# Kernel tuning notes

Measured on AMD Instinct MI355X. Metric: run time of the kernel, lower is better.

The kernel has to match this reference:

```python
import jax, jax.numpy as jnp
import numpy as np

PT_SEQ_LEN = 16    # hardcoded hw_seq_len in the module
THETA = 10000.0


def _rope_tables(head_dim):
    # VisionRotaryEmbeddingFast with dim = head_dim // 2, pt_seq_len = ft_seq_len = 16
    d = head_dim // 2                                   # 32
    freqs = 1.0 / (THETA ** (np.arange(0, d, 2, dtype=np.float64) / d))  # (d//2,) = (16,)
    t = np.arange(PT_SEQ_LEN, dtype=np.float64)         # t / ft * pt = arange since ft==pt
    f = np.einsum('i,j->ij', t, freqs)                  # (16, 16)
    f = np.repeat(f, 2, axis=-1)                        # (16, 32)  '... n -> ... (n r)'
    fa = np.broadcast_to(f[:, None, :], (PT_SEQ_LEN, PT_SEQ_LEN, d))
    fb = np.broadcast_to(f[None, :, :], (PT_SEQ_LEN, PT_SEQ_LEN, d))
    full = np.concatenate([fa, fb], axis=-1).reshape(-1, head_dim)  # (256, head_dim)
    return (jnp.asarray(np.cos(full), dtype=jnp.float32),
            jnp.asarray(np.sin(full), dtype=jnp.float32))


def _rotate_half(x):
    # '... (d r) -> ... d r', r=2; (x1, x2) -> (-x2, x1)
    x = x.reshape(*x.shape[:-1], -1, 2)
    x1, x2 = x[..., 0], x[..., 1]
    return jnp.stack((-x2, x1), axis=-1).reshape(*x.shape[:-2], -1)


def _apply_rope(t, cos, sin):
    # t: (B, H, N, hd); cos/sin: (N, hd)
    return t * cos + _rotate_half(t) * sin


def setup_inputs() -> dict:
    key = jax.random.key(0)
    ks = jax.random.split(key, 5)
    B, N, dim, sem = 64, 256, 1024, 768
    return {
        'q': jax.random.normal(ks[0], (B, N, dim), dtype=jnp.float32),
        'kv': jax.random.normal(ks[1], (B, N, sem), dtype=jnp.float32),
        'Wq': jax.random.normal(ks[2], (dim, dim), dtype=jnp.float32) * 0.02,
        'Wkv': jax.random.normal(ks[3], (sem, 2 * dim), dtype=jnp.float32) * 0.02,
        'Wproj': jax.random.normal(ks[4], (dim, dim), dtype=jnp.float32) * 0.02,
        'bproj': jnp.zeros((dim,), dtype=jnp.float32),
    }


def reference(q, kv, Wq, Wkv, Wproj, bproj):
    B, N, C = q.shape
    H = 16
    hd = C // H
    cos, sin = _rope_tables(hd)

    qh = (q @ Wq).reshape(B, N, H, hd).transpose(0, 2, 1, 3)        # (B,H,N,hd)
    kvh = (kv @ Wkv).reshape(B, N, 2, H, hd).transpose(2, 0, 3, 1, 4)
    k, v = kvh[0], kvh[1]                                           # (B,H,N,hd)

    qh = _apply_rope(qh, cos, sin)
    k = _apply_rope(k, cos, sin)

    scale = 1.0 / jnp.sqrt(jnp.float32(hd))  # F.sdpa default scale
    logits = jnp.einsum('bhqd,bhkd->bhqk', qh, k) * scale
    attn = jax.nn.softmax(logits, axis=-1)
    out = jnp.einsum('bhqk,bhkd->bhqd', attn, v)                    # (B,H,N,hd)
    out = out.transpose(0, 2, 1, 3).reshape(B, N, C)
    return out @ Wproj + bproj
```

## Files before the change

### kernel.cpp

```cpp
#include <hip/hip_runtime.h>
#include <hip/hip_bf16.h>
#include <math.h>


typedef unsigned int uint;
typedef __attribute__((ext_vector_type(4)))  short s16x4;
typedef __attribute__((ext_vector_type(8)))  short s16x8;
typedef __attribute__((ext_vector_type(4)))  float f32x4;

#define AS1 __attribute__((address_space(1)))
#define AS3 __attribute__((address_space(3)))

__device__ __forceinline__ short f2bf(float x){
  union{float f;uint u;}v; v.f=x;
  return (short)((v.u + 0x7FFFu + ((v.u>>16)&1u))>>16);
}
__device__ __forceinline__ float bf2f(short s){
  union{float f;uint u;}v; v.u=((uint)(unsigned short)s)<<16; return v.f;
}
__device__ __forceinline__ uint packbf(float a,float b){
  return (uint)(unsigned short)f2bf(a) | ((uint)(unsigned short)f2bf(b)<<16);
}
__device__ __forceinline__ void gl_lds16(const void* g, void* l){
  __builtin_amdgcn_global_load_lds((const AS1 uint*)g, (AS3 uint*)l, 16, 0, 0);
}
__device__ __forceinline__ s16x8 ld16(const short* p){ return *(const s16x8*)p; }

__global__ void k_detect(const uint* q, int* flag){
  __shared__ int cnt;
  if(threadIdx.x==0) cnt=0;
  __syncthreads();
  int c=0;
  for(int i=threadIdx.x;i<4096;i+=256){
    uint e=(q[i]>>7)&0xFFu;
    if(e>=120u && e<=130u) c++;
  }
  atomicAdd(&cnt,c);
  __syncthreads();
  if(threadIdx.x==0) *flag = (cnt>2048)?0:1;
}

__global__ void k_convert(const void* src, short* dst, long n8, const int* flag){
  int f=*flag;
  long stride=(long)gridDim.x*blockDim.x;
  for(long i=(long)blockIdx.x*blockDim.x+threadIdx.x;i<n8;i+=stride){
    s16x8 o;
    if(f){
      const float4* s=(const float4*)src;
      float4 a=s[i*2], b=s[i*2+1];
      o[0]=f2bf(a.x);o[1]=f2bf(a.y);o[2]=f2bf(a.z);o[3]=f2bf(a.w);
      o[4]=f2bf(b.x);o[5]=f2bf(b.y);o[6]=f2bf(b.z);o[7]=f2bf(b.w);
    }else{
      o=((const s16x8*)src)[i];
    }
    ((s16x8*)dst)[i]=o;
  }
}

__global__ void k_transpose(const void* W, short* WT, int K, int Nn, const int* flag){
  int f=*flag;
  long total=(long)Nn*(K/8);
  long stride=(long)gridDim.x*blockDim.x;
  for(long idx=(long)blockIdx.x*blockDim.x+threadIdx.x;idx<total;idx+=stride){
    int n=(int)(idx%Nn); int kc=(int)(idx/Nn); int k0=kc*8;
    s16x8 o;
    #pragma unroll
    for(int j=0;j<8;j++){
      o[j]= f ? f2bf(((const float*)W)[(long)(k0+j)*Nn+n])
              : ((const short*)W)[(long)(k0+j)*Nn+n];
    }
    *(s16x8*)&WT[(long)n*K+k0]=o;
  }
}

__global__ void k_tables(float* cosT, float* sinT){
  int t=blockIdx.x*blockDim.x+threadIdx.x;
  if(t>=256*64) return;
  int n=t>>6, d=t&63;
  int i=n>>4, j=n&15;
  int p=(d&31)>>1;
  double fr=pow(10000.0, -(double)(2*p)/32.0);
  double tt=(d<32)?(double)i:(double)j;
  double a=tt*fr;
  cosT[t]=(float)cos(a);
  sinT[t]=(float)sin(a);
}

__global__ void k_bias(const void* b, float* bo, const int* flag){
  int t=blockIdx.x*blockDim.x+threadIdx.x;
  if(t<1024) bo[t] = (*flag)? ((const float*)b)[t] : bf2f(((const short*)b)[t]);
}

template<int EPI>
__launch_bounds__(256,2)
__global__ void k_gemm(const short* A, const short* BT, int Kdim,
                       short* out0, short* out1,
                       const float* cosT, const float* sinT,
                       const float* bias, const int* flag, void* dout){
  __shared__ __align__(16) short Alds[2][128*32];
  __shared__ __align__(16) short Blds[2][128*32];
  const int tid=threadIdx.x, lane=tid&63;
  const int wave=tid>>6, wm=wave>>1, wn=wave&1;
  const int tn=blockIdx.x, tm=blockIdx.y;
  const int fl=*flag;
  f32x4 acc[4][4]={};
  const short* Ag=A+(long)tm*128*Kdim;
  const short* Bg=BT+(long)tn*128*Kdim;
  const int row0=tid>>2, c0=tid&3;
  const int row1=64+row0;
  const int sw0=(c0^((row0>>1)&3))*8;
  const int sw1=(c0^((row1>>1)&3))*8;

  #define STAGE(bufsel,kb) do{                                        \
    gl_lds16(Ag+(long)row0*Kdim+(kb)+sw0, &Alds[bufsel][tid*8]);      \
    gl_lds16(Ag+(long)row1*Kdim+(kb)+sw1, &Alds[bufsel][(256+tid)*8]);\
    gl_lds16(Bg+(long)row0*Kdim+(kb)+sw0, &Blds[bufsel][tid*8]);      \
    gl_lds16(Bg+(long)row1*Kdim+(kb)+sw1, &Blds[bufsel][(256+tid)*8]);\
  }while(0)

  const int nt=Kdim>>5;
  STAGE(0,0);
  __syncthreads();
  int cur=0;
  for(int t=0;t<nt;t++){
    if(t+1<nt) STAGE(cur^1,(t+1)*32);
    s16x8 af[4], bfr[4];
    #pragma unroll
    for(int rb=0;rb<4;rb++){
      int ar=wm*64+rb*16+(lane&15);
      af[rb]=*(const s16x8*)&Alds[cur][ar*32+(((lane>>4)^((ar>>1)&3))*8)];
    }
    #pragma unroll
    for(int cb=0;cb<4;cb++){
      int br=wn*64+cb*16+(lane&15);
      bfr[cb]=*(const s16x8*)&Blds[cur][br*32+(((lane>>4)^((br>>1)&3))*8)];
    }
    #pragma unroll
    for(int rb=0;rb<4;rb++)
      #pragma unroll
      for(int cb=0;cb<4;cb++)
        acc[rb][cb]=__builtin_amdgcn_mfma_f32_16x16x32_bf16(af[rb],bfr[cb],acc[rb][cb],0,0,0);
    __syncthreads();
    cur^=1;
  }
  #undef STAGE

  const int mbase=tm*128+wm*64, nbase=tn*128+wn*64;
  const int g=lane>>4, li=lane&15;
  #pragma unroll
  for(int rb=0;rb<4;rb++)
  #pragma unroll
  for(int cb=0;cb<4;cb++){
    const int m0=mbase+rb*16+g*4;
    const int n=nbase+cb*16+li;
    if(EPI==0){
      #pragma unroll
      for(int r=0;r<4;r++){
        float v=acc[rb][cb][r];
        int m=m0+r; int b=m>>8, nn=m&255, h=n>>6, d=n&63;
        float part=__shfl_xor(v,1);
        float c=cosT[(nn<<6)+d], s=sinT[(nn<<6)+d];
        float rot=(d&1)?part:-part;
        out0[(((long)(b*16+h)*256+nn)<<6)+d]=f2bf((v*c+rot*s)*0.125f);
      }
    } else if(EPI==1){
      if(n<1024){
        #pragma unroll
        for(int r=0;r<4;r++){
          float v=acc[rb][cb][r];
          int m=m0+r; int b=m>>8, nn=m&255, h=(n>>6)&15, d=n&63;
          float part=__shfl_xor(v,1);
          float c=cosT[(nn<<6)+d], s=sinT[(nn<<6)+d];
          float rot=(d&1)?part:-part;
          out0[(((long)(b*16+h)*256+nn)<<6)+d]=f2bf(v*c+rot*s);
        }
      }else{
        int h=(n>>6)&15, d=n&63;
        int b=m0>>8, nn0=m0&255;
        s16x4 pk;
        #pragma unroll
        for(int r=0;r<4;r++) pk[r]=f2bf(acc[rb][cb][r]);
        *(s16x4*)&out1[(((long)(b*16+h)*64+d)<<8)+nn0]=pk;
      }
    } else {
      #pragma unroll
      for(int r=0;r<4;r++){
        float o=acc[rb][cb][r]+bias[n];
        long idx=((long)(m0+r)<<10)+n;
        if(fl) ((float*)dout)[idx]=o;
        else   ((short*)dout)[idx]=f2bf(o);
      }
    }
  }
}

__launch_bounds__(256,2)
__global__ void k_attn(const short* qh, const short* kb, const short* vt, short* out){
  __shared__ __align__(16) short ol[4][64][72];
  int bh=blockIdx.x, b=bh>>4, h=bh&15;
  int tid=threadIdx.x, lane=tid&63, wave=tid>>6;
  const short* Q=qh+(long)bh*256*64;
  const short* K=kb+(long)bh*256*64;
  const short* VT=vt+(long)bh*64*256;

  s16x8 qf[4][2];
  #pragma unroll
  for(int qb=0;qb<4;qb++)
    #pragma unroll
    for(int kk=0;kk<2;kk++)
      qf[qb][kk]=ld16(Q+(wave*64+qb*16+(lane&15))*64+kk*32+(lane>>4)*8);

  f32x4 o[4][4]={};
  float mrow[4]={-INFINITY,-INFINITY,-INFINITY,-INFINITY};
  float srow[4]={0.f,0.f,0.f,0.f};
  const int g=lane>>4;
  const int srcA=(lane&15)|((((g<<1))&3)<<4);
  const int srcB=(lane&15)|((((g<<1)|1)&3)<<4);
  const bool hi=(g>=2);

  for(int kt=0;kt<8;kt++){
    s16x8 kA[2][2];
    #pragma unroll
    for(int f=0;f<2;f++)
      #pragma unroll
      for(int kk=0;kk<2;kk++)
        kA[f][kk]=ld16(K+(kt*32+f*16+(lane&15))*64+kk*32+(lane>>4)*8);
    f32x4 st[2][4]={};
    #pragma unroll
    for(int kk=0;kk<2;kk++)
      #pragma unroll
      for(int f=0;f<2;f++)
        #pragma unroll
        for(int qb=0;qb<4;qb++)
          st[f][qb]=__builtin_amdgcn_mfma_f32_16x16x32_bf16(kA[f][kk],qf[qb][kk],st[f][qb],0,0,0);

    s16x8 pb[4];
    #pragma unroll
    for(int qb=0;qb<4;qb++){
      float pm=st[0][qb][0];
      #pragma unroll
      for(int f=0;f<2;f++)
        #pragma unroll
        for(int r=0;r<4;r++) pm=fmaxf(pm,st[f][qb][r]);
      pm=fmaxf(pm,__shfl_xor(pm,16));
      pm=fmaxf(pm,__shfl_xor(pm,32));
      float mn=fmaxf(mrow[qb],pm);
      float al=__expf(mrow[qb]-mn);
      mrow[qb]=mn;
      float p00=__expf(st[0][qb][0]-mn), p01=__expf(st[0][qb][1]-mn);
      float p02=__expf(st[0][qb][2]-mn), p03=__expf(st[0][qb][3]-mn);
      float p10=__expf(st[1][qb][0]-mn), p11=__expf(st[1][qb][1]-mn);
      float p12=__expf(st[1][qb][2]-mn), p13=__expf(st[1][qb][3]-mn);
      float ps=p00+p01+p02+p03+p10+p11+p12+p13;
      ps+=__shfl_xor(ps,16);
      ps+=__shfl_xor(ps,32);
      srow[qb]=srow[qb]*al+ps;
      #pragma unroll
      for(int db=0;db<4;db++){
        o[db][qb][0]*=al; o[db][qb][1]*=al; o[db][qb][2]*=al; o[db][qb][3]*=al;
      }
      uint pk00=packbf(p00,p01), pk01=packbf(p02,p03);
      uint pk10=packbf(p10,p11), pk11=packbf(p12,p13);
      uint s00=(uint)__shfl((int)pk00,srcA), s10=(uint)__shfl((int)pk10,srcA);
      uint s01=(uint)__shfl((int)pk01,srcA), s11=(uint)__shfl((int)pk11,srcA);
      uint t00=(uint)__shfl((int)pk00,srcB), t10=(uint)__shfl((int)pk10,srcB);
      uint t01=(uint)__shfl((int)pk01,srcB), t11=(uint)__shfl((int)pk11,srcB);
      union{s16x8 v;uint u[4];}pp;
      pp.u[0]=hi?s10:s00;
      pp.u[1]=hi?s11:s01;
      pp.u[2]=hi?t10:t00;
      pp.u[3]=hi?t11:t01;
      pb[qb]=pp.v;
    }
    s16x8 vA[4];
    #pragma unroll
    for(int db=0;db<4;db++)
      vA[db]=ld16(VT+(db*16+(lane&15))*256+kt*32+(lane>>4)*8);
    #pragma unroll
    for(int db=0;db<4;db++)
      #pragma unroll
      for(int qb=0;qb<4;qb++)
        o[db][qb]=__builtin_amdgcn_mfma_f32_16x16x32_bf16(vA[db],pb[qb],o[db][qb],0,0,0);
  }

  #pragma unroll
  for(int db=0;db<4;db++)
    #pragma unroll
    for(int qb=0;qb<4;qb++)
      #pragma unroll
      for(int r=0;r<4;r++){
        int d=db*16+(lane>>4)*4+r;
        int q=qb*16+(lane&15);
        ol[wave][q][d]=f2bf(o[db][qb][r]/srow[qb]);
      }
  __syncthreads();
  #pragma unroll
  for(int it=0;it<8;it++){
    int q=wave*64+it*8+(lane>>3);
    int cc=lane&7;
    s16x8 x=*(const s16x8*)&ol[wave][it*8+(lane>>3)][cc*8];
    *(s16x8*)&out[((long)(b*256+q)<<10)+h*64+cc*8]=x;
  }
}

extern "C" void kernel_launch(void* const* d_in, const int* in_sizes, int n_in,
                              void* d_out, int out_size, void* d_ws, size_t ws_size,
                              hipStream_t stream){
  const long M=16384;
  char* ws=(char*)d_ws;
  size_t off=0;
  auto alloc=[&](size_t b){ void* p=ws+off; off+=(b+255)&~(size_t)255; return p; };
  int*   flag =(int*)  alloc(256);
  float* cosT =(float*)alloc(256*64*4);
  float* sinT =(float*)alloc(256*64*4);
  float* biasF=(float*)alloc(1024*4);
  short* qbf  =(short*)alloc((size_t)M*1024*2);
  short* kvbf =(short*)alloc((size_t)M*768*2);
  short* WqT  =(short*)alloc((size_t)1024*1024*2);
  short* WkvT =(short*)alloc((size_t)2048*768*2);
  short* WpT  =(short*)alloc((size_t)1024*1024*2);
  short* qhB  =(short*)alloc((size_t)16777216*2);
  short* kbuf =(short*)alloc((size_t)16777216*2);
  short* vtb  =(short*)alloc((size_t)16777216*2);

  k_detect<<<1,256,0,stream>>>((const uint*)d_in[0],flag);
  k_tables<<<64,256,0,stream>>>(cosT,sinT);
  k_bias<<<4,256,0,stream>>>(d_in[5],biasF,flag);
  k_convert<<<2048,256,0,stream>>>(d_in[0],qbf,(long)M*1024/8,flag);
  k_convert<<<2048,256,0,stream>>>(d_in[1],kvbf,(long)M*768/8,flag);
  k_transpose<<<512,256,0,stream>>>(d_in[2],WqT,1024,1024,flag);
  k_transpose<<<768,256,0,stream>>>(d_in[3],WkvT,768,2048,flag);
  k_transpose<<<512,256,0,stream>>>(d_in[4],WpT,1024,1024,flag);

  k_gemm<0><<<dim3(8,128),256,0,stream>>>(qbf ,WqT ,1024,qhB ,nullptr,cosT,sinT,biasF,flag,nullptr);
  k_gemm<1><<<dim3(16,128),256,0,stream>>>(kvbf,WkvT, 768,kbuf,vtb    ,cosT,sinT,biasF,flag,nullptr);
  k_attn<<<1024,256,0,stream>>>(qhB,kbuf,vtb,qbf);
  k_gemm<2><<<dim3(8,128),256,0,stream>>>(qbf ,WpT ,1024,nullptr,nullptr,cosT,sinT,biasF,flag,d_out);
}
```

Baseline: 310.6 us.

## Replace GEMM with 256x256-tile 8-wave ping-pong pipelined kernel

Replaces the 128x128, 4-wave, K=32 double-buffered GEMM with a 256x256-tile, 8-wave kernel that uses K=64 stages. Global-to-LDS loads of the next tiles are interleaved with MFMA quarter-blocks, using explicit barriers, waitcnt and s_setprio. Workgroups are remapped across the 8 XCDs for L2 locality. The aim is to raise data reuse per LDS byte and overlap memory traffic with compute. In exchange it adds much higher register pressure (128 accumulators per lane), fragile hand-written synchronisation, and a wraparound prefetch past the last K tile.

```diff
diff --git a/kernel.cpp b/kernel.cpp
--- a/kernel.cpp
+++ b/kernel.cpp
@@ -6,6 +6,7 @@
 typedef unsigned int uint;
 typedef __attribute__((ext_vector_type(4)))  short s16x4;
 typedef __attribute__((ext_vector_type(8)))  short s16x8;
+typedef __attribute__((ext_vector_type(16))) short s16x16;
 typedef __attribute__((ext_vector_type(4)))  float f32x4;
 
 #define AS1 __attribute__((address_space(1)))
@@ -91,73 +92,115 @@
   if(t<1024) bo[t] = (*flag)? ((const float*)b)[t] : bf2f(((const short*)b)[t]);
 }
 
+#define BAR   __builtin_amdgcn_s_barrier()
+#define LGKM0 asm volatile("s_waitcnt lgkmcnt(0)" ::: "memory")
+#define VMC4  asm volatile("s_waitcnt vmcnt(4)" ::: "memory")
+#define PRIO1 __builtin_amdgcn_s_setprio(1)
+#define PRIO0 __builtin_amdgcn_s_setprio(0)
+
+#define MM(H,V,BR) do{ \
+  _Pragma("unroll") for(int ks_=0;ks_<2;ks_++){ \
+    _Pragma("unroll") for(int mf_=0;mf_<4;mf_++){ \
+      _Pragma("unroll") for(int nf_=0;nf_<2;nf_++){ \
+        acc[(H)*4+mf_][(V)*2+nf_]=__builtin_amdgcn_mfma_f32_16x16x32_bf16( \
+          aR[mf_][ks_],BR[nf_][ks_],acc[(H)*4+mf_][(V)*2+nf_],0,0,0); \
+  }}} }while(0)
+
+#define HALFIT(BUF,TA,TB) do{ \
+  const short* RA=&lds[BUF][0][wm][0]; \
+  const short* RB=&lds[BUF][1][0][0]; \
+  ldA(RA,0,aR); ldB(RB,0,bR0); stage(0,0,TA); \
+  BAR; LGKM0; PRIO1; MM(0,0,bR0); PRIO0; BAR; \
+  ldB(RB,1,bR1); stage(0,1,TA); \
+  BAR; LGKM0; PRIO1; MM(0,1,bR1); PRIO0; BAR; \
+  ldA(RA,1,aR); stage(1,0,TB); \
+  BAR; LGKM0; PRIO1; MM(1,1,bR1); PRIO0; BAR; \
+  stage(1,1,TB); \
+  BAR; PRIO1; MM(1,0,bR0); PRIO0; VMC4; BAR; \
+}while(0)
+
 template<int EPI>
-__launch_bounds__(256,2)
-__global__ void k_gemm(const short* A, const short* BT, int Kdim,
-                       short* out0, short* out1,
-                       const float* cosT, const float* sinT,
-                       const float* bias, const int* flag, void* dout){
-  __shared__ __align__(16) short Alds[2][128*32];
-  __shared__ __align__(16) short Blds[2][128*32];
-  const int tid=threadIdx.x, lane=tid&63;
-  const int wave=tid>>6, wm=wave>>1, wn=wave&1;
-  const int tn=blockIdx.x, tm=blockIdx.y;
-  const int fl=*flag;
-  f32x4 acc[4][4]={};
-  const short* Ag=A+(long)tm*128*Kdim;
-  const short* Bg=BT+(long)tn*128*Kdim;
-  const int row0=tid>>2, c0=tid&3;
-  const int row1=64+row0;
-  const int sw0=(c0^((row0>>1)&3))*8;
-  const int sw1=(c0^((row1>>1)&3))*8;
-
-  #define STAGE(bufsel,kb) do{                                        \
-    gl_lds16(Ag+(long)row0*Kdim+(kb)+sw0, &Alds[bufsel][tid*8]);      \
-    gl_lds16(Ag+(long)row1*Kdim+(kb)+sw1, &Alds[bufsel][(256+tid)*8]);\
-    gl_lds16(Bg+(long)row0*Kdim+(kb)+sw0, &Blds[bufsel][tid*8]);      \
-    gl_lds16(Bg+(long)row1*Kdim+(kb)+sw1, &Blds[bufsel][(256+tid)*8]);\
-  }while(0)
-
-  const int nt=Kdim>>5;
-  STAGE(0,0);
-  __syncthreads();
-  int cur=0;
-  for(int t=0;t<nt;t++){
-    if(t+1<nt) STAGE(cur^1,(t+1)*32);
-    s16x8 af[4], bfr[4];
-    #pragma unroll
-    for(int rb=0;rb<4;rb++){
-      int ar=wm*64+rb*16+(lane&15);
-      af[rb]=*(const s16x8*)&Alds[cur][ar*32+(((lane>>4)^((ar>>1)&3))*8)];
-    }
-    #pragma unroll
-    for(int cb=0;cb<4;cb++){
-      int br=wn*64+cb*16+(lane&15);
-      bfr[cb]=*(const s16x8*)&Blds[cur][br*32+(((lane>>4)^((br>>1)&3))*8)];
-    }
-    #pragma unroll
-    for(int rb=0;rb<4;rb++)
-      #pragma unroll
-      for(int cb=0;cb<4;cb++)
-        acc[rb][cb]=__builtin_amdgcn_mfma_f32_16x16x32_bf16(af[rb],bfr[cb],acc[rb][cb],0,0,0);
-    __syncthreads();
-    cur^=1;
-  }
-  #undef STAGE
-
-  const int mbase=tm*128+wm*64, nbase=tn*128+wn*64;
-  const int g=lane>>4, li=lane&15;
-  #pragma unroll
-  for(int rb=0;rb<4;rb++)
-  #pragma unroll
-  for(int cb=0;cb<4;cb++){
-    const int m0=mbase+rb*16+g*4;
-    const int n=nbase+cb*16+li;
+__launch_bounds__(512,2)
+__global__ void k_gemm8(const short* __restrict__ A, const short* __restrict__ BT,
+                        const int Kdim, const int lgN,
+                        short* __restrict__ out0, short* __restrict__ out1,
+                        const float* __restrict__ cosT, const float* __restrict__ sinT,
+                        const float* __restrict__ bias, const int* __restrict__ flag,
+                        void* __restrict__ dout){
+  __shared__ __align__(16) short lds[2][2][2][8192];
+  const int tid=threadIdx.x, lane=tid&63, wave=tid>>6;
+  const int li=lane&15, gq=lane>>4;
+  const int wm=wave>>2, wn=wave&3;
+  const int nwg=gridDim.x, cpx=nwg>>3;
+  const int wg=((int)blockIdx.x&7)*cpx+((int)blockIdx.x>>3);
+  const int tn=wg&((1<<lgN)-1), tm=wg>>lgN;
+  const int NT=Kdim>>6;
+  const short* Ag=A+(long)tm*256*Kdim;
+  const short* Bg=BT+(long)tn*256*Kdim;
+  const int fl=(EPI==2)? *flag : 0;
+  f32x4 acc[8][4]={};
+  s16x8 aR[4][2], bR0[2][2], bR1[2][2];
+
+  auto stage=[&](int op,int hf,int kt){
+    int ktw=(kt>=NT)?kt-NT:kt;
+    const short* G=(op? Bg:Ag)+((long)(hf*128))*Kdim+ktw*64;
+    short* R=&lds[kt&1][op][hf][0];
+    #pragma unroll
+    for(int l=0;l<2;l++){
+      int lr=l*64+wave*8+(lane>>3);
+      int c=(lane&7)^((lr>>1)&7);
+      gl_lds16(G+(long)lr*Kdim+c*8, R+l*4096+wave*512+lane*8);
+    }
+  };
+  auto ldA=[&](const short* R,int h,s16x8 (&a)[4][2]){
+    #pragma unroll
+    for(int mf=0;mf<4;mf++){
+      int lr=(h*4+mf)*16+li;
+      int sw=(lr>>1)&7;
+      #pragma unroll
+      for(int ks=0;ks<2;ks++){
+        int slot=(ks*4+gq)^sw;
+        a[mf][ks]=*(const s16x8*)&R[lr*64+slot*8];
+      }
+    }
+  };
+  auto ldB=[&](const short* R0,int v,s16x8 (&b)[2][2]){
+    #pragma unroll
+    for(int nf=0;nf<2;nf++){
+      int row=wn*64+(v*2+nf)*16+li;
+      const short* R=R0+(row>>7)*8192;
+      int lr=row&127;
+      int sw=(lr>>1)&7;
+      #pragma unroll
+      for(int ks=0;ks<2;ks++){
+        int slot=(ks*4+gq)^sw;
+        b[nf][ks]=*(const s16x8*)&R[lr*64+slot*8];
+      }
+    }
+  };
+
+  stage(1,0,0); stage(1,1,0); stage(0,0,0); stage(0,1,0);
+  stage(1,0,1); stage(1,1,1);
+  VMC4;
+  BAR;
+
+  for(int t=0;t<NT;t+=2){
+    HALFIT(0, t+1, t+2);
+    HALFIT(1, t+2, t+3);
+  }
+
+  const int mb=tm*256+wm*128, nb=tn*256+wn*64;
+  #pragma unroll
+  for(int mf=0;mf<8;mf++)
+  #pragma unroll
+  for(int nf=0;nf<4;nf++){
+    const int m0=mb+mf*16+gq*4;
+    const int n=nb+nf*16+li;
     if(EPI==0){
       #pragma unroll
       for(int r=0;r<4;r++){
-        float v=acc[rb][cb][r];
-        int m=m0+r; int b=m>>8, nn=m&255, h=n>>6, d=n&63;
+        float v=acc[mf][nf][r];
+        int m=m0+r, b=m>>8, nn=m&255, h=n>>6, d=n&63;
         float part=__shfl_xor(v,1);
         float c=cosT[(nn<<6)+d], s=sinT[(nn<<6)+d];
         float rot=(d&1)?part:-part;
@@ -167,25 +210,24 @@
       if(n<1024){
         #pragma unroll
         for(int r=0;r<4;r++){
-          float v=acc[rb][cb][r];
-          int m=m0+r; int b=m>>8, nn=m&255, h=(n>>6)&15, d=n&63;
+          float v=acc[mf][nf][r];
+          int m=m0+r, b=m>>8, nn=m&255, h=(n>>6)&15, d=n&63;
           float part=__shfl_xor(v,1);
           float c=cosT[(nn<<6)+d], s=sinT[(nn<<6)+d];
           float rot=(d&1)?part:-part;
           out0[(((long)(b*16+h)*256+nn)<<6)+d]=f2bf(v*c+rot*s);
         }
       }else{
-        int h=(n>>6)&15, d=n&63;
-        int b=m0>>8, nn0=m0&255;
+        int h=(n>>6)&15, d=n&63, b=m0>>8, nn0=m0&255;
         s16x4 pk;
         #pragma unroll
-        for(int r=0;r<4;r++) pk[r]=f2bf(acc[rb][cb][r]);
+        for(int r=0;r<4;r++) pk[r]=f2bf(acc[mf][nf][r]);
         *(s16x4*)&out1[(((long)(b*16+h)*64+d)<<8)+nn0]=pk;
       }
     } else {
       #pragma unroll
       for(int r=0;r<4;r++){
-        float o=acc[rb][cb][r]+bias[n];
+        float o=acc[mf][nf][r]+bias[n];
         long idx=((long)(m0+r)<<10)+n;
         if(fl) ((float*)dout)[idx]=o;
         else   ((short*)dout)[idx]=f2bf(o);
@@ -332,8 +374,8 @@
   k_transpose<<<768,256,0,stream>>>(d_in[3],WkvT,768,2048,flag);
   k_transpose<<<512,256,0,stream>>>(d_in[4],WpT,1024,1024,flag);
 
-  k_gemm<0><<<dim3(8,128),256,0,stream>>>(qbf ,WqT ,1024,qhB ,nullptr,cosT,sinT,biasF,flag,nullptr);
-  k_gemm<1><<<dim3(16,128),256,0,stream>>>(kvbf,WkvT, 768,kbuf,vtb    ,cosT,sinT,biasF,flag,nullptr);
+  k_gemm8<0><<<256,512,0,stream>>>(qbf ,WqT ,1024,2,qhB ,nullptr,cosT,sinT,biasF,flag,nullptr);
+  k_gemm8<1><<<512,512,0,stream>>>(kvbf,WkvT, 768,3,kbuf,vtb    ,cosT,sinT,biasF,flag,nullptr);
   k_attn<<<1024,256,0,stream>>>(qhB,kbuf,vtb,qbf);
-  k_gemm<2><<<dim3(8,128),256,0,stream>>>(qbf ,WpT ,1024,nullptr,nullptr,cosT,sinT,biasF,flag,d_out);
-}
+  k_gemm8<2><<<256,512,0,stream>>>(qbf ,WpT ,1024,2,nullptr,nullptr,cosT,sinT,biasF,flag,d_out);
+}
```

New measurement: 270.8 us. -12.8%, faster.
